# Optimization experiments

Hardware: AMD Instinct MI355X
Metric: run time of the kernel (lower is better)

Reference implementation:

```python
import jax, jax.numpy as jnp
import numpy as np

B, D, K = 64, 8732, 81
RATIO = 1.0

def setup_inputs() -> dict:
    key = jax.random.key(0)
    k1, k2, k3, k4 = jax.random.split(key, 4)
    return {
        'loc_preds': jax.random.normal(k1, (B, D, 4), dtype=jnp.float32),
        'loc_targets': jax.random.normal(k2, (B, D, 4), dtype=jnp.float32),
        'conf_preds': jax.random.normal(k3, (B, D, K), dtype=jnp.float32),
        'conf_targets': jax.random.randint(k4, (B, D), 0, K, dtype=jnp.int32),
    }

def reference(loc_preds, loc_targets, conf_preds, conf_targets):
    b, d, k = conf_preds.shape
    pos = conf_targets > 0                                  # [B, D] bool
    num_matched = jnp.sum(pos).astype(conf_preds.dtype)     # scalar (python float in torch)
    num_matched = jax.lax.stop_gradient(num_matched)

    # --- localization smooth-L1 over positive boxes only ---
    z = jnp.abs(loc_preds - loc_targets)
    sl1 = jnp.where(z < 1.0, 0.5 * z * z, z - 0.5)          # [B, D, 4]
    loc_loss = jnp.sum(sl1 * pos[..., None].astype(sl1.dtype))

    # --- per-box CE (custom: GLOBAL max for stability), detached, for mining ---
    x = conf_preds.reshape(-1, k)                           # [B*D, K]
    y = conf_targets.reshape(-1)                            # [B*D]
    xmax = jnp.max(x)                                       # x.data.max() in torch (global scalar)
    lse = jnp.log(jnp.sum(jnp.exp(x - xmax), axis=1)) + xmax
    ce_mine = lse - jnp.take_along_axis(x, y[:, None].astype(jnp.int32), axis=1)[:, 0]
    conf_loss_mat = jax.lax.stop_gradient(ce_mine).reshape(b, d)

    # --- hard negative mining: double argsort rank trick ---
    cl = jnp.where(pos, 0.0, conf_loss_mat)                 # conf_loss[pos] = 0
    idx = jnp.argsort(-cl, axis=1)                          # descending sort indices
    rank = jnp.argsort(idx, axis=1)                         # rank of each box
    num_pos = jnp.sum(pos, axis=1, keepdims=True).astype(jnp.float32)   # [B,1]
    num_neg = jnp.minimum(3.0 * RATIO * num_pos, float(d - 1))          # clamp max=D-1
    neg = rank.astype(jnp.float32) < num_neg                # [B, D] bool

    # --- final confidence loss: standard CE summed over pos | neg ---
    sel = (pos | neg).reshape(-1)                           # [B*D]
    logp = jax.nn.log_softmax(x, axis=1)
    ce = -jnp.take_along_axis(logp, y[:, None].astype(jnp.int32), axis=1)[:, 0]
    conf_loss = jnp.sum(jnp.where(sel, ce, 0.0))

    loc_loss = loc_loss / num_matched
    conf_loss = conf_loss / num_matched
    return (loc_loss + conf_loss, conf_loss, loc_loss)
```

## Files before the change

kernel.cpp:

```cpp
#include <hip/hip_runtime.h>
#include <math.h>

constexpr int BB = 64;
constexpr int DD = 8732;
constexpr int KK = 81;
constexpr int BPB = 256;
constexpr int SL = (DD + BPB - 1) / BPB;
constexpr int NPART = BB * SL;

typedef float f4 __attribute__((ext_vector_type(4)));

__device__ inline float smooth_l1(float d) {
    float z = fabsf(d);
    return z < 1.0f ? 0.5f * z * z : z - 0.5f;
}

__device__ inline float sel4(f4 v, int comp) {
    return (comp == 0) ? v.x : (comp == 1) ? v.y : (comp == 2) ? v.z : v.w;
}

__global__ void __launch_bounds__(1024) fused_kernel(
    const f4* __restrict__ lp, const f4* __restrict__ lt,
    const float* __restrict__ cp, const int* __restrict__ ct,
    int* __restrict__ cnt_part, float* __restrict__ ce_part,
    float* __restrict__ loc_part)
{
    int tid = threadIdx.x;
    int slice = blockIdx.x, row = blockIdx.y;
    int bir = slice * BPB + (tid >> 2);
    int q = tid & 3;
    float ce_c = 0.0f, locs = 0.0f;
    int c = 0;
    if (bir < DD) {
        size_t g = (size_t)row * DD + bir;
        const float* rowp = cp + g * KK;
        const f4* r4 = (const f4*)rowp;
        f4 f[5];
        #pragma unroll
        for (int t = 0; t < 5; ++t) f[t] = r4[q + 4 * t];
        f4 fx = f[0];
        if (q == 3) fx = *(const f4*)(rowp + 77);
        int y = ct[g];

        float m = -INFINITY;
        #pragma unroll
        for (int t = 0; t < 5; ++t)
            m = fmaxf(m, fmaxf(fmaxf(f[t].x, f[t].y), fmaxf(f[t].z, f[t].w)));
        if (q == 3) m = fmaxf(m, fx.w);
        m = fmaxf(m, __shfl_xor(m, 1));
        m = fmaxf(m, __shfl_xor(m, 2));

        float s = 0.0f;
        #pragma unroll
        for (int t = 0; t < 5; ++t)
            s += __expf(f[t].x - m) + __expf(f[t].y - m)
               + __expf(f[t].z - m) + __expf(f[t].w - m);
        if (q == 3) s += __expf(fx.w - m);
        s += __shfl_xor(s, 1);
        s += __shfl_xor(s, 2);

        int yt = y >> 4, comp = y & 3;
        f4 fy = (yt == 0) ? f[0] : (yt == 1) ? f[1] : (yt == 2) ? f[2]
              : (yt == 3) ? f[3] : f[4];
        float cand = sel4(fy, comp);
        if (y == 80) cand = fx.w;
        int lane = tid & 63;
        int src = (lane & ~3) | ((y == 80) ? 3 : ((y >> 2) & 3));
        float xv = __shfl(cand, src);

        if (q == 0) ce_c = __logf(s) + m - xv;
        if (q == 1 && y > 0) {
            c = 1;
            f4 a = lp[g], b = lt[g];
            locs = smooth_l1(a.x - b.x) + smooth_l1(a.y - b.y)
                 + smooth_l1(a.z - b.z) + smooth_l1(a.w - b.w);
        }
    }
    for (int o = 32; o; o >>= 1) {
        locs += __shfl_down(locs, o);
        ce_c += __shfl_down(ce_c, o);
        c    += __shfl_down(c, o);
    }
    __shared__ float s_l[16], s_e[16];
    __shared__ int   s_c[16];
    int lane = tid & 63, wid = tid >> 6;
    if (lane == 0) { s_l[wid] = locs; s_e[wid] = ce_c; s_c[wid] = c; }
    __syncthreads();
    if (tid == 0) {
        float L = 0.0f, E = 0.0f; int C = 0;
        #pragma unroll
        for (int k = 0; k < 16; ++k) { L += s_l[k]; E += s_e[k]; C += s_c[k]; }
        int idx = row * SL + slice;
        loc_part[idx] = L;
        ce_part[idx]  = E;
        cnt_part[idx] = C;
    }
}

__global__ void __launch_bounds__(1024) finish_kernel(
    const int* __restrict__ cnt_part, const float* __restrict__ ce_part,
    const float* __restrict__ loc_part, const float* __restrict__ cp,
    const int* __restrict__ ct, float* __restrict__ out)
{
    __shared__ int s_np[BB];
    __shared__ double s_ce[BB];
    __shared__ double s_l[16], s_n[16], s_fs[16];
    __shared__ double s_conf;
    __shared__ int s_fb[BB], s_nfb;
    __shared__ float cl[DD];

    int tid = threadIdx.x;
    int lane = tid & 63, wid = tid >> 6;
    int row = tid >> 4, sub = tid & 15;

    int np = 0; double ces = 0.0;
    for (int s = sub; s < SL; s += 16) {
        int idx = row * SL + s;
        np += cnt_part[idx];
        ces += (double)ce_part[idx];
    }
    for (int o = 8; o; o >>= 1) { np += __shfl_down(np, o); ces += __shfl_down(ces, o); }
    if (sub == 0) { s_np[row] = np; s_ce[row] = ces; }

    double l = 0.0, n = 0.0;
    for (int j = tid; j < NPART; j += 1024) {
        l += (double)loc_part[j];
        n += (double)cnt_part[j];
    }
    for (int o = 32; o; o >>= 1) { l += __shfl_down(l, o); n += __shfl_down(n, o); }
    if (lane == 0) { s_l[wid] = l; s_n[wid] = n; }
    __syncthreads();

    if (tid == 0) {
        double conf = 0.0; int nfb = 0;
        for (int r = 0; r < BB; ++r) {
            float numneg = fminf(3.0f * (float)s_np[r], (float)(DD - 1));
            int M = DD - s_np[r];
            if ((float)M <= numneg) conf += s_ce[r];
            else s_fb[nfb++] = r;
        }
        s_conf = conf; s_nfb = nfb;
    }
    __syncthreads();

    for (int fi = 0; fi < s_nfb; ++fi) {
        int r = s_fb[fi];
        float numneg = fminf(3.0f * (float)s_np[r], (float)(DD - 1));
        const int* ctr = ct + r * DD;
        const float* base = cp + (size_t)r * DD * KK;
        double sum = 0.0;
        for (int i = tid; i < DD; i += 1024) {
            const float* rowp = base + (size_t)i * KK;
            float m = -INFINITY;
            for (int k = 0; k < KK; ++k) m = fmaxf(m, rowp[k]);
            float s = 0.0f;
            for (int k = 0; k < KK; ++k) s += __expf(rowp[k] - m);
            float cei = __logf(s) + m - rowp[ctr[i]];
            if (ctr[i] > 0) { sum += (double)cei; cl[i] = 0.0f; }
            else cl[i] = cei;
        }
        __syncthreads();
        for (int i = tid; i < DD; i += 1024) {
            if (ctr[i] > 0) continue;
            float ci = cl[i];
            int rk = 0;
            for (int j = 0; j < DD; j++) {
                float cj = cl[j];
                rk += (cj > ci || (cj == ci && j < i)) ? 1 : 0;
            }
            if ((float)rk < numneg) sum += (double)ci;
        }
        for (int o = 32; o; o >>= 1) sum += __shfl_down(sum, o);
        if (lane == 0) s_fs[wid] = sum;
        __syncthreads();
        if (tid == 0) {
            double t = 0.0;
            for (int k = 0; k < 16; ++k) t += s_fs[k];
            s_conf += t;
        }
        __syncthreads();
    }

    if (tid == 0) {
        double L = 0.0, N = 0.0;
        for (int k = 0; k < 16; ++k) { L += s_l[k]; N += s_n[k]; }
        double C = s_conf;
        out[0] = (float)(L / N + C / N);
        out[1] = (float)(C / N);
        out[2] = (float)(L / N);
    }
}

extern "C" void kernel_launch(void* const* d_in, const int* in_sizes, int n_in,
                              void* d_out, int out_size, void* d_ws, size_t ws_size,
                              hipStream_t stream) {
    const f4* lp = (const f4*)d_in[0];
    const f4* lt = (const f4*)d_in[1];
    const float* cp = (const float*)d_in[2];
    const int* ct = (const int*)d_in[3];
    float* out = (float*)d_out;

    char* w = (char*)d_ws;
    int*   cnt_part = (int*)w;
    float* loc_part = (float*)(w + 9216);
    float* ce_part  = (float*)(w + 18432);

    dim3 grid(SL, BB);
    fused_kernel<<<grid, 1024, 0, stream>>>(lp, lt, cp, ct,
                                            cnt_part, ce_part, loc_part);
    finish_kernel<<<1, 1024, 0, stream>>>(cnt_part, ce_part, loc_part, cp, ct, out);
}
```

Before: 46.09 us.

## Loop each block over multiple box chunks with register double-buffered prefetch

The fused kernel now uses 256-thread blocks, and each block processes 8 chunks of 64 boxes. Loads for the next chunk are issued into registers before the current chunk is computed, and per-thread accumulators carry across iterations. This aims to hide global-memory latency with software prefetching and to cut the number of blocks and partial sums. The cost is higher register pressure from the doubled buffers, and fewer blocks in flight, which may lower occupancy on a bandwidth-bound kernel.

```diff
diff --git a/kernel.cpp b/kernel.cpp
--- a/kernel.cpp
+++ b/kernel.cpp
@@ -4,8 +4,10 @@
 constexpr int BB = 64;
 constexpr int DD = 8732;
 constexpr int KK = 81;
-constexpr int BPB = 256;
-constexpr int SL = (DD + BPB - 1) / BPB;
+constexpr int CHUNK = 64;
+constexpr int NITER = 8;
+constexpr int BOXPB = CHUNK * NITER;
+constexpr int SL = (DD + BOXPB - 1) / BOXPB;
 constexpr int NPART = BB * SL;
 
 typedef float f4 __attribute__((ext_vector_type(4)));
@@ -19,81 +21,106 @@
     return (comp == 0) ? v.x : (comp == 1) ? v.y : (comp == 2) ? v.z : v.w;
 }
 
-__global__ void __launch_bounds__(1024) fused_kernel(
+__global__ void __launch_bounds__(256) fused_kernel(
     const f4* __restrict__ lp, const f4* __restrict__ lt,
     const float* __restrict__ cp, const int* __restrict__ ct,
     int* __restrict__ cnt_part, float* __restrict__ ce_part,
     float* __restrict__ loc_part)
 {
     int tid = threadIdx.x;
-    int slice = blockIdx.x, row = blockIdx.y;
-    int bir = slice * BPB + (tid >> 2);
+    int sg = blockIdx.x, row = blockIdx.y;
     int q = tid & 3;
-    float ce_c = 0.0f, locs = 0.0f;
-    int c = 0;
-    if (bir < DD) {
+    int base = sg * BOXPB + (tid >> 2);
+    int lane = tid & 63;
+
+    float ce_acc = 0.0f, loc_acc = 0.0f;
+    int c_acc = 0;
+
+    int bir = base;
+    bool act = bir < DD;
+    f4 cur[5] = {}; f4 curx = {}; int ycur = 0; f4 cla = {}, clb = {};
+    if (act) {
         size_t g = (size_t)row * DD + bir;
         const float* rowp = cp + g * KK;
         const f4* r4 = (const f4*)rowp;
-        f4 f[5];
         #pragma unroll
-        for (int t = 0; t < 5; ++t) f[t] = r4[q + 4 * t];
-        f4 fx = f[0];
-        if (q == 3) fx = *(const f4*)(rowp + 77);
-        int y = ct[g];
-
-        float m = -INFINITY;
+        for (int t = 0; t < 5; ++t) cur[t] = r4[q + 4 * t];
+        if (q == 3) curx = *(const f4*)(rowp + 77);
+        ycur = ct[g];
+        if (q == 1) { cla = lp[g]; clb = lt[g]; }
+    }
+
+    #pragma unroll
+    for (int it = 0; it < NITER; ++it) {
+        int nbir = base + (it + 1) * CHUNK;
+        bool nact = (it + 1 < NITER) && (nbir < DD);
+        f4 nxt[5] = {}; f4 nxtx = {}; int ynxt = 0; f4 nla = {}, nlb = {};
+        if (nact) {
+            size_t g = (size_t)row * DD + nbir;
+            const float* rowp = cp + g * KK;
+            const f4* r4 = (const f4*)rowp;
+            #pragma unroll
+            for (int t = 0; t < 5; ++t) nxt[t] = r4[q + 4 * t];
+            if (q == 3) nxtx = *(const f4*)(rowp + 77);
+            ynxt = ct[g];
+            if (q == 1) { nla = lp[g]; nlb = lt[g]; }
+        }
+        if (act) {
+            float m = -INFINITY;
+            #pragma unroll
+            for (int t = 0; t < 5; ++t)
+                m = fmaxf(m, fmaxf(fmaxf(cur[t].x, cur[t].y),
+                                   fmaxf(cur[t].z, cur[t].w)));
+            if (q == 3) m = fmaxf(m, curx.w);
+            m = fmaxf(m, __shfl_xor(m, 1));
+            m = fmaxf(m, __shfl_xor(m, 2));
+
+            float s = 0.0f;
+            #pragma unroll
+            for (int t = 0; t < 5; ++t)
+                s += __expf(cur[t].x - m) + __expf(cur[t].y - m)
+                   + __expf(cur[t].z - m) + __expf(cur[t].w - m);
+            if (q == 3) s += __expf(curx.w - m);
+            s += __shfl_xor(s, 1);
+            s += __shfl_xor(s, 2);
+
+            int y = ycur;
+            int yt = y >> 4, comp = y & 3;
+            f4 fy = (yt == 0) ? cur[0] : (yt == 1) ? cur[1] : (yt == 2) ? cur[2]
+                  : (yt == 3) ? cur[3] : cur[4];
+            float cand = sel4(fy, comp);
+            if (y == 80) cand = curx.w;
+            int src = (lane & ~3) | ((y == 80) ? 3 : ((y >> 2) & 3));
+            float xv = __shfl(cand, src);
+
+            if (q == 0) ce_acc += __logf(s) + m - xv;
+            if (q == 1 && y > 0) {
+                c_acc += 1;
+                loc_acc += smooth_l1(cla.x - clb.x) + smooth_l1(cla.y - clb.y)
+                         + smooth_l1(cla.z - clb.z) + smooth_l1(cla.w - clb.w);
+            }
+        }
+        act = nact;
         #pragma unroll
-        for (int t = 0; t < 5; ++t)
-            m = fmaxf(m, fmaxf(fmaxf(f[t].x, f[t].y), fmaxf(f[t].z, f[t].w)));
-        if (q == 3) m = fmaxf(m, fx.w);
-        m = fmaxf(m, __shfl_xor(m, 1));
-        m = fmaxf(m, __shfl_xor(m, 2));
-
-        float s = 0.0f;
-        #pragma unroll
-        for (int t = 0; t < 5; ++t)
-            s += __expf(f[t].x - m) + __expf(f[t].y - m)
-               + __expf(f[t].z - m) + __expf(f[t].w - m);
-        if (q == 3) s += __expf(fx.w - m);
-        s += __shfl_xor(s, 1);
-        s += __shfl_xor(s, 2);
-
-        int yt = y >> 4, comp = y & 3;
-        f4 fy = (yt == 0) ? f[0] : (yt == 1) ? f[1] : (yt == 2) ? f[2]
-              : (yt == 3) ? f[3] : f[4];
-        float cand = sel4(fy, comp);
-        if (y == 80) cand = fx.w;
-        int lane = tid & 63;
-        int src = (lane & ~3) | ((y == 80) ? 3 : ((y >> 2) & 3));
-        float xv = __shfl(cand, src);
-
-        if (q == 0) ce_c = __logf(s) + m - xv;
-        if (q == 1 && y > 0) {
-            c = 1;
-            f4 a = lp[g], b = lt[g];
-            locs = smooth_l1(a.x - b.x) + smooth_l1(a.y - b.y)
-                 + smooth_l1(a.z - b.z) + smooth_l1(a.w - b.w);
-        }
-    }
+        for (int t = 0; t < 5; ++t) cur[t] = nxt[t];
+        curx = nxtx; ycur = ynxt; cla = nla; clb = nlb;
+    }
+
     for (int o = 32; o; o >>= 1) {
-        locs += __shfl_down(locs, o);
-        ce_c += __shfl_down(ce_c, o);
-        c    += __shfl_down(c, o);
-    }
-    __shared__ float s_l[16], s_e[16];
-    __shared__ int   s_c[16];
-    int lane = tid & 63, wid = tid >> 6;
-    if (lane == 0) { s_l[wid] = locs; s_e[wid] = ce_c; s_c[wid] = c; }
+        loc_acc += __shfl_down(loc_acc, o);
+        ce_acc  += __shfl_down(ce_acc, o);
+        c_acc   += __shfl_down(c_acc, o);
+    }
+    __shared__ float s_l[4], s_e[4];
+    __shared__ int   s_c[4];
+    int wid = tid >> 6;
+    if (lane == 0) { s_l[wid] = loc_acc; s_e[wid] = ce_acc; s_c[wid] = c_acc; }
     __syncthreads();
     if (tid == 0) {
-        float L = 0.0f, E = 0.0f; int C = 0;
-        #pragma unroll
-        for (int k = 0; k < 16; ++k) { L += s_l[k]; E += s_e[k]; C += s_c[k]; }
-        int idx = row * SL + slice;
-        loc_part[idx] = L;
-        ce_part[idx]  = E;
-        cnt_part[idx] = C;
+        int idx = row * SL + sg;
+        loc_part[idx] = s_l[0] + s_l[1] + s_l[2] + s_l[3];
+        ce_part[idx]  = s_e[0] + s_e[1] + s_e[2] + s_e[3];
+        cnt_part[idx] = s_c[0] + s_c[1] + s_c[2] + s_c[3];
     }
 }
 
@@ -202,11 +229,11 @@
 
     char* w = (char*)d_ws;
     int*   cnt_part = (int*)w;
-    float* loc_part = (float*)(w + 9216);
-    float* ce_part  = (float*)(w + 18432);
+    float* loc_part = (float*)(w + 8192);
+    float* ce_part  = (float*)(w + 16384);
 
     dim3 grid(SL, BB);
-    fused_kernel<<<grid, 1024, 0, stream>>>(lp, lt, cp, ct,
-                                            cnt_part, ce_part, loc_part);
+    fused_kernel<<<grid, 256, 0, stream>>>(lp, lt, cp, ct,
+                                           cnt_part, ce_part, loc_part);
     finish_kernel<<<1, 1024, 0, stream>>>(cnt_part, ce_part, loc_part, cp, ct, out);
 }
```

New measurement: 49.12 us. 1.07x slower.
